# Optimization experiments

Measured on AMD Instinct MI355X. Metric: run time of the kernel, lower is better.

Reference implementation:

```python
import jax, jax.numpy as jnp
import numpy as np

HIDDEN = 2048
NUM_HEADS = 16
NUM_KV_HEADS = 4
HEAD_DIM = HIDDEN // NUM_HEADS  # 128
ROPE_THETA = 1000000.0
B, S = 2, 2048


def setup_inputs() -> dict:
    key = jax.random.key(0)
    ks = jax.random.split(key, 10)
    sc = 0.02
    return {
        "hidden_states": jax.random.normal(ks[0], (B, S, HIDDEN), jnp.float32),
        "position_ids": jnp.broadcast_to(jnp.arange(S, dtype=jnp.int32), (B, S)),
        "Wq": jax.random.normal(ks[1], (HIDDEN, NUM_HEADS * HEAD_DIM), jnp.float32) * sc,
        "bq": jnp.zeros((NUM_HEADS * HEAD_DIM,), jnp.float32),
        "Wk": jax.random.normal(ks[2], (HIDDEN, NUM_KV_HEADS * HEAD_DIM), jnp.float32) * sc,
        "bk": jnp.zeros((NUM_KV_HEADS * HEAD_DIM,), jnp.float32),
        "Wv": jax.random.normal(ks[3], (HIDDEN, NUM_KV_HEADS * HEAD_DIM), jnp.float32) * sc,
        "bv": jnp.zeros((NUM_KV_HEADS * HEAD_DIM,), jnp.float32),
        "Wo": jax.random.normal(ks[4], (NUM_HEADS * HEAD_DIM, HIDDEN), jnp.float32) * sc,
        "bo": jnp.zeros((HIDDEN,), jnp.float32),
    }


def _rope_cos_sin(position_ids, dtype):
    # inv_freq: [head_dim/2]
    inv_freq = 1.0 / (ROPE_THETA ** (jnp.arange(0, HEAD_DIM, 2, dtype=jnp.float32) / HEAD_DIM))
    freqs = position_ids.astype(jnp.float32)[:, :, None] * inv_freq[None, None, :]  # [B,S,d/2]
    emb = jnp.concatenate([freqs, freqs], axis=-1)  # [B,S,d]
    return jnp.cos(emb).astype(dtype), jnp.sin(emb).astype(dtype)


def _rotate_half(x):
    h = x.shape[-1] // 2
    return jnp.concatenate([-x[..., h:], x[..., :h]], axis=-1)


def _attention(hidden_states, position_ids, Wq, bq, Wk, bk, Wv, bv, Wo, bo):
    bsz, q_len, _ = hidden_states.shape
    q = (hidden_states @ Wq + bq).reshape(bsz, q_len, NUM_HEADS, HEAD_DIM).transpose(0, 2, 1, 3)
    k = (hidden_states @ Wk + bk).reshape(bsz, q_len, NUM_KV_HEADS, HEAD_DIM).transpose(0, 2, 1, 3)
    v = (hidden_states @ Wv + bv).reshape(bsz, q_len, NUM_KV_HEADS, HEAD_DIM).transpose(0, 2, 1, 3)

    cos, sin = _rope_cos_sin(position_ids, hidden_states.dtype)
    cos = cos[:, None, :, :]  # [B,1,S,d]
    sin = sin[:, None, :, :]
    q = q * cos + _rotate_half(q) * sin
    k = k * cos + _rotate_half(k) * sin

    # repeat_kv (GQA): [B,kvh,S,d] -> [B,H,S,d]
    n_rep = NUM_HEADS // NUM_KV_HEADS
    k = jnp.repeat(k, n_rep, axis=1)
    v = jnp.repeat(v, n_rep, axis=1)

    scale = 1.0 / jnp.sqrt(jnp.array(HEAD_DIM, hidden_states.dtype))
    scores = jnp.einsum('bhqd,bhkd->bhqk', q, k) * scale  # [B,H,S,S]
    causal = jnp.tril(jnp.ones((q_len, q_len), bool))
    scores = jnp.where(causal[None, None], scores, jnp.finfo(scores.dtype).min)
    probs = jax.nn.softmax(scores.astype(jnp.float32), axis=-1).astype(hidden_states.dtype)
    attn = jnp.einsum('bhqk,bhkd->bhqd', probs, v)
    attn = attn.transpose(0, 2, 1, 3).reshape(bsz, q_len, HIDDEN)
    return attn @ Wo + bo


def reference(hidden_states, position_ids, Wq, bq, Wk, bk, Wv, bv, Wo, bo):
    return _attention(hidden_states, position_ids, Wq, bq, Wk, bk, Wv, bv, Wo, bo)
```

## Files before the change

kernel.cpp:

```cpp
#include <hip/hip_runtime.h>
#include <cmath>

#define HIDDEN 2048
#define NH 16
#define NKV 4
#define HD 128
#define SEQ 2048
#define BATCH 2

typedef unsigned short ushort_t;
typedef short bf16x8 __attribute__((ext_vector_type(8)));
typedef float f32x4 __attribute__((ext_vector_type(4)));
typedef ushort_t u16x4 __attribute__((ext_vector_type(4)));

__device__ __forceinline__ ushort_t f2bf(float f) {
    union { float f; unsigned int u; } v; v.f = f;
    unsigned int r = v.u + 0x7fffu + ((v.u >> 16) & 1u);
    return (ushort_t)(r >> 16);
}
__device__ __forceinline__ ushort_t f2bf_trunc(float f) {
    union { float f; unsigned int u; } v; v.f = f;
    return (ushort_t)(v.u >> 16);
}

__device__ __forceinline__ f32x4 mfma16(bf16x8 a, bf16x8 b, f32x4 c) {
    return __builtin_amdgcn_mfma_f32_16x16x32_bf16(a, b, c, 0, 0, 0);
}

__device__ __forceinline__ void load_lds16(const void* g, void* l) {
    __builtin_amdgcn_global_load_lds((const __attribute__((address_space(1))) unsigned int*)g,
                                     (__attribute__((address_space(3))) unsigned int*)l,
                                     16, 0, 0);
}

__global__ __launch_bounds__(256) void convert_x(const float* __restrict__ x,
                                                 ushort_t* __restrict__ xb, int n4) {
    int g = blockIdx.x * 256 + threadIdx.x;
    if (g >= n4) return;
    float4 v = ((const float4*)x)[g];
    u16x4 o;
    o[0] = f2bf(v.x); o[1] = f2bf(v.y); o[2] = f2bf(v.z); o[3] = f2bf(v.w);
    ((u16x4*)xb)[g] = o;
}

__global__ __launch_bounds__(256) void transpose_all(const float* __restrict__ Wq,
                                                     const float* __restrict__ Wk,
                                                     const float* __restrict__ Wv,
                                                     const float* __restrict__ Wo,
                                                     ushort_t* __restrict__ WqkvT,
                                                     ushort_t* __restrict__ WoT) {
    const int z = blockIdx.z;
    const float* W;
    ushort_t* WT;
    int N;
    if (z == 0)      { W = Wq; WT = WqkvT;                        N = 2048; }
    else if (z == 1) { W = Wk; WT = WqkvT + 2048ull * 2048;       N = 512;  }
    else if (z == 2) { W = Wv; WT = WqkvT + 2560ull * 2048;       N = 512;  }
    else             { W = Wo; WT = WoT;                          N = 2048; }
    const int K = 2048;
    const int n0 = blockIdx.x * 64, k0 = blockIdx.y * 64;
    if (n0 >= N) return;
    __shared__ ushort_t T[64][72];
    const int t = threadIdx.x;
    for (int idx = t; idx < 64 * 16; idx += 256) {
        int r = idx >> 4, c4 = (idx & 15) << 2;
        float4 v = *(const float4*)&W[(size_t)(k0 + r) * N + n0 + c4];
        T[r][c4 + 0] = f2bf(v.x); T[r][c4 + 1] = f2bf(v.y);
        T[r][c4 + 2] = f2bf(v.z); T[r][c4 + 3] = f2bf(v.w);
    }
    __syncthreads();
    for (int idx = t; idx < 64 * 16; idx += 256) {
        int n = idx >> 4, kg = (idx & 15) << 2;
        u16x4 o;
        o[0] = T[kg + 0][n]; o[1] = T[kg + 1][n];
        o[2] = T[kg + 2][n]; o[3] = T[kg + 3][n];
        *(u16x4*)&WT[(size_t)(n0 + n) * K + k0 + kg] = o;
    }
}

template <int MODE, int BMH>
__global__ __launch_bounds__(512) void gemm256(const ushort_t* __restrict__ A,
                                               const ushort_t* __restrict__ Bt,
                                               const float* __restrict__ bias,
                                               const float* __restrict__ bias2,
                                               const float* __restrict__ bias3,
                                               void* __restrict__ out,
                                               void* __restrict__ out2,
                                               void* __restrict__ out3,
                                               int M, int N, int K,
                                               const int* __restrict__ posids) {
    constexpr int IM = 4 * BMH;
    __shared__ __align__(16) ushort_t Asb[2][BMH * 8192];
    __shared__ __align__(16) ushort_t Bsb[2][16384];
    const int tid = threadIdx.x;
    const int w = tid >> 6, lane = tid & 63, quad = lane >> 4, l16 = lane & 15;
    const int wr = w >> 2, wc = w & 3;
    const int m0 = blockIdx.y * (128 * BMH), n0 = blockIdx.x * 256;

    f32x4 acc[IM][4];
#pragma unroll
    for (int i = 0; i < IM; i++)
#pragma unroll
        for (int j = 0; j < 4; j++)
#pragma unroll
            for (int e = 0; e < 4; e++) acc[i][j][e] = 0.0f;

    const int lrow = lane >> 3;
    const int kh_s = ((lane >> 2) & 1) ^ ((lane >> 3) & 1);
    const int c_s  = (lane & 3) ^ ((lane >> 4) & 3);
    const int scol = kh_s * 32 + c_s * 8;

    auto stageA = [&](int t, int buf, int ha) {
        const ushort_t* g = A + (size_t)(m0 + ha * 128 + w * 16 + lrow) * K + t * 64 + scol;
        ushort_t* l = &Asb[buf][(ha * 128 + w * 16) * 64];
        load_lds16(g, l);
        load_lds16(g + (size_t)8 * K, l + 512);
    };
    auto stageB = [&](int t, int buf, int ha) {
        const ushort_t* g = Bt + (size_t)(n0 + ha * 128 + w * 16 + lrow) * K + t * 64 + scol;
        ushort_t* l = &Bsb[buf][(ha * 128 + w * 16) * 64];
        load_lds16(g, l);
        load_lds16(g + (size_t)8 * K, l + 512);
    };

    const int sw = (quad ^ ((l16 >> 1) & 3)) * 8;
    const int off0 = ((l16 & 1) ? 32 : 0) + sw;
    const int off1 = ((l16 & 1) ? 0 : 32) + sw;
    const int arow = (wr * (64 * BMH) + l16) * 64;
    const int brow = (wc * 16 + l16) * 64;

    const int nt = K >> 6;

    stageA(0, 0, 0);
    if constexpr (BMH == 2) stageA(0, 0, 1);
    stageB(0, 0, 0);
    stageB(0, 0, 1);
    asm volatile("s_waitcnt vmcnt(2)" ::: "memory");
    __builtin_amdgcn_s_barrier();
    __builtin_amdgcn_sched_barrier(0);

    bf16x8 a[IM];
    for (int u = 0; u < nt; ++u) {
        const int bu = u & 1, bn = bu ^ 1;
        const bool pf = (u + 1 < nt);
        const ushort_t* Ab = Asb[bu];
        const ushort_t* Bb = Bsb[bu];

#pragma unroll
        for (int i = 0; i < IM; i++) a[i] = *(const bf16x8*)&Ab[arow + i * 1024 + off0];
        bf16x8 b0 = *(const bf16x8*)&Bb[brow + off0];
        bf16x8 b1 = *(const bf16x8*)&Bb[brow + 4096 + off0];
        if (pf) { stageA(u + 1, bn, 0); asm volatile("s_waitcnt vmcnt(2)" ::: "memory"); }
        else    { asm volatile("s_waitcnt vmcnt(0)" ::: "memory"); }
        __builtin_amdgcn_s_barrier();
        __builtin_amdgcn_sched_barrier(0);
        __builtin_amdgcn_s_setprio(1);
#pragma unroll
        for (int i = 0; i < IM; i++) {
            acc[i][0] = mfma16(a[i], b0, acc[i][0]);
            acc[i][1] = mfma16(a[i], b1, acc[i][1]);
        }
        __builtin_amdgcn_s_setprio(0);
        __builtin_amdgcn_sched_barrier(0);
        __builtin_amdgcn_s_barrier();
        __builtin_amdgcn_sched_barrier(0);

        bf16x8 b2 = *(const bf16x8*)&Bb[brow + 8192 + off0];
        bf16x8 b3 = *(const bf16x8*)&Bb[brow + 12288 + off0];
        if (pf) {
            if constexpr (BMH == 2) stageA(u + 1, bn, 1);
            else                    stageB(u + 1, bn, 0);
        }
        __builtin_amdgcn_s_barrier();
        __builtin_amdgcn_sched_barrier(0);
        __builtin_amdgcn_s_setprio(1);
#pragma unroll
        for (int i = 0; i < IM; i++) {
            acc[i][2] = mfma16(a[i], b2, acc[i][2]);
            acc[i][3] = mfma16(a[i], b3, acc[i][3]);
        }
        __builtin_amdgcn_s_setprio(0);
        __builtin_amdgcn_sched_barrier(0);
        __builtin_amdgcn_s_barrier();
        __builtin_amdgcn_sched_barrier(0);

#pragma unroll
        for (int i = 0; i < IM; i++) a[i] = *(const bf16x8*)&Ab[arow + i * 1024 + off1];
        b0 = *(const bf16x8*)&Bb[brow + off1];
        b1 = *(const bf16x8*)&Bb[brow + 4096 + off1];
        if (pf) {
            if constexpr (BMH == 2) stageB(u + 1, bn, 0);
            else                    stageB(u + 1, bn, 1);
        }
        __builtin_amdgcn_s_barrier();
        __builtin_amdgcn_sched_barrier(0);
        __builtin_amdgcn_s_setprio(1);
#pragma unroll
        for (int i = 0; i < IM; i++) {
            acc[i][0] = mfma16(a[i], b0, acc[i][0]);
            acc[i][1] = mfma16(a[i], b1, acc[i][1]);
        }
        __builtin_amdgcn_s_setprio(0);
        __builtin_amdgcn_sched_barrier(0);
        __builtin_amdgcn_s_barrier();
        __builtin_amdgcn_sched_barrier(0);

        b2 = *(const bf16x8*)&Bb[brow + 8192 + off1];
        b3 = *(const bf16x8*)&Bb[brow + 12288 + off1];
        if (pf) {
            if constexpr (BMH == 2) stageB(u + 1, bn, 1);
            asm volatile("s_waitcnt vmcnt(2)" ::: "memory");
        }
        __builtin_amdgcn_s_barrier();
        __builtin_amdgcn_sched_barrier(0);
        __builtin_amdgcn_s_setprio(1);
#pragma unroll
        for (int i = 0; i < IM; i++) {
            acc[i][2] = mfma16(a[i], b2, acc[i][2]);
            acc[i][3] = mfma16(a[i], b3, acc[i][3]);
        }
        __builtin_amdgcn_s_setprio(0);
        __builtin_amdgcn_sched_barrier(0);
        __builtin_amdgcn_s_barrier();
        __builtin_amdgcn_sched_barrier(0);
    }

    if (MODE == 0) {
        float* O = (float*)out;
#pragma unroll
        for (int i = 0; i < IM; i++)
#pragma unroll
            for (int r = 0; r < 4; r++) {
                int row = m0 + wr * (64 * BMH) + i * 16 + quad * 4 + r;
#pragma unroll
                for (int j = 0; j < 4; j++) {
                    int col = n0 + (wc + 4 * j) * 16 + l16;
                    O[(size_t)row * N + col] = acc[i][j][r] + bias[col];
                }
            }
    } else {
        if (n0 < 2048) {
            ushort_t* O = (ushort_t*)out;
            const int h0 = n0 >> 7;
            const float scale = 0.08838834764831845f;
            const int dl = wc * 16 + l16;
            const float fr = __expf(-0.21586735246819178f * (float)dl);
#pragma unroll
            for (int i = 0; i < IM; i++)
#pragma unroll
                for (int r = 0; r < 4; r++) {
                    int row = m0 + wr * (64 * BMH) + i * 16 + quad * 4 + r;
                    int b = row >> 11, s = row & (SEQ - 1);
                    float pos = (float)posids[row];
                    float sn, cs;
                    __sincosf(pos * fr, &sn, &cs);
#pragma unroll
                    for (int p = 0; p < 2; p++) {
                        float x1 = acc[i][2 * p][r] + bias[n0 + p * 128 + dl];
                        float x2 = acc[i][2 * p + 1][r] + bias[n0 + p * 128 + dl + 64];
                        size_t obase = ((size_t)(b * NH + h0 + p) * SEQ + s) * HD;
                        O[obase + dl]      = f2bf((x1 * cs - x2 * sn) * scale);
                        O[obase + dl + 64] = f2bf((x2 * cs + x1 * sn) * scale);
                    }
                }
        } else if (n0 < 2560) {
            ushort_t* O = (ushort_t*)out2;
            const int n0k = n0 - 2048;
            const int h0 = n0k >> 7;
            const int dl = wc * 16 + l16;
            const float fr = __expf(-0.21586735246819178f * (float)dl);
#pragma unroll
            for (int i = 0; i < IM; i++)
#pragma unroll
                for (int r = 0; r < 4; r++) {
                    int row = m0 + wr * (64 * BMH) + i * 16 + quad * 4 + r;
                    int b = row >> 11, s = row & (SEQ - 1);
                    float pos = (float)posids[row];
                    float sn, cs;
                    __sincosf(pos * fr, &sn, &cs);
#pragma unroll
                    for (int p = 0; p < 2; p++) {
                        float x1 = acc[i][2 * p][r] + bias2[n0k + p * 128 + dl];
                        float x2 = acc[i][2 * p + 1][r] + bias2[n0k + p * 128 + dl + 64];
                        size_t obase = ((size_t)(b * NKV + h0 + p) * SEQ + s) * HD;
                        O[obase + dl]      = f2bf(x1 * cs - x2 * sn);
                        O[obase + dl + 64] = f2bf(x2 * cs + x1 * sn);
                    }
                }
        } else {
            ushort_t* O = (ushort_t*)out3;
            const int n0v = n0 - 2560;
#pragma unroll
            for (int i = 0; i < IM; i++)
#pragma unroll
                for (int r = 0; r < 4; r++) {
                    int row = m0 + wr * (64 * BMH) + i * 16 + quad * 4 + r;
                    int b = row >> 11, s = row & (SEQ - 1);
#pragma unroll
                    for (int j = 0; j < 4; j++) {
                        int ct = wc + 4 * j;
                        int h = (n0v >> 7) + (ct >> 3);
                        int d = (ct & 7) * 16 + l16;
                        float v = acc[i][j][r] + bias3[n0v + ct * 16 + l16];
                        O[((size_t)(b * NKV + h) * HD + d) * SEQ + s] = f2bf(v);
                    }
                }
        }
    }
}

__global__ __launch_bounds__(256) void flash(const ushort_t* __restrict__ Qr,
                                             const ushort_t* __restrict__ Kr,
                                             const ushort_t* __restrict__ Vt,
                                             ushort_t* __restrict__ Attn) {
    __shared__ __align__(16) ushort_t Ksh[2 * 4 * 64 * 32];
    __shared__ __align__(16) ushort_t Vsh[2 * 2 * 128 * 32];
    __shared__ __align__(16) ushort_t Ps[4 * 16 * 72];
    const int tid = threadIdx.x;
    const int w = tid >> 6, lane = tid & 63, quad = lane >> 4, l16 = lane & 15;
    const int x = blockIdx.x, h = blockIdx.y, b = blockIdx.z;
    const int qa = x, qb = 31 - x;
    const int nkt = qb + 1;
    const int hkv = h >> 2;
    const ushort_t* Kg = Kr + ((size_t)(b * NKV + hkv) * SEQ) * HD;
    const ushort_t* Vg = Vt + ((size_t)(b * NKV + hkv) * HD) * SEQ;

    const int p = lane >> 2;
    const int gc8 = (((lane & 3) ^ ((lane >> 3) & 3)) << 3);
    const ushort_t* kst = Kg + (size_t)p * HD + w * 32 + gc8;
    const ushort_t* vst = Vg + (size_t)((w & 1) * 64 + p) * SEQ + (w >> 1) * 32 + gc8;
    ushort_t* ksl = Ksh + w * 2048;
    ushort_t* vsl = Vsh + (w >> 1) * 4096 + (w & 1) * 2048;

    auto stage = [&](int bi, int kv0) {
        const ushort_t* gk = kst + (size_t)kv0 * HD;
        ushort_t* lk = ksl + bi * 8192;
        load_lds16(gk, lk);
        load_lds16(gk + (size_t)16 * HD, lk + 512);
        load_lds16(gk + (size_t)32 * HD, lk + 1024);
        load_lds16(gk + (size_t)48 * HD, lk + 1536);
        const ushort_t* gv = vst + kv0;
        ushort_t* lv = vsl + bi * 8192;
        load_lds16(gv, lv);
        load_lds16(gv + (size_t)16 * SEQ, lv + 512);
        load_lds16(gv + (size_t)32 * SEQ, lv + 1024);
        load_lds16(gv + (size_t)48 * SEQ, lv + 1536);
    };

    bf16x8 aq[2][4];
#pragma unroll
    for (int st = 0; st < 2; st++) {
        const int qst = st ? qb : qa;
        const size_t qrow = ((size_t)(b * NH + h) * SEQ + qst * 64 + w * 16 + l16) * HD;
#pragma unroll
        for (int kc = 0; kc < 4; kc++)
            aq[st][kc] = *(const bf16x8*)&Qr[qrow + kc * 32 + quad * 8];
    }

    f32x4 o[2][8];
#pragma unroll
    for (int st = 0; st < 2; st++)
#pragma unroll
        for (int j = 0; j < 8; j++)
#pragma unroll
            for (int e = 0; e < 4; e++) o[st][j][e] = 0.0f;
    f32x4 ls2[2];
#pragma unroll
    for (int st = 0; st < 2; st++)
        for (int e = 0; e < 4; e++) ls2[st][e] = 0.0f;
    bf16x8 ones;
#pragma unroll
    for (int e = 0; e < 8; e++) ones[e] = (short)0x3F80;

    ushort_t* Pw = &Ps[w * 16 * 72];
    const int rsw8 = ((l16 >> 1) & 3) << 3;

    stage(0, 0);
    asm volatile("s_waitcnt vmcnt(0)" ::: "memory");
    __builtin_amdgcn_s_barrier();

    for (int kt = 0; kt < nkt; kt++) {
        const int kv0 = kt * 64;
        const int cur = kt & 1;
        if (kt + 1 < nkt) {
            stage(cur ^ 1, kv0 + 64);
            asm volatile("s_waitcnt vmcnt(8)" ::: "memory");
        } else {
            asm volatile("s_waitcnt vmcnt(0)" ::: "memory");
        }
        __builtin_amdgcn_s_barrier();

        const ushort_t* Kb = Ksh + cur * 8192;
        const ushort_t* Vb = Vsh + cur * 8192;

#pragma unroll
        for (int st = 0; st < 2; st++) {
            const int qst = st ? qb : qa;
            if (st == 0 && kt > qa) continue;

            f32x4 sa[4];
#pragma unroll
            for (int nt = 0; nt < 4; nt++)
#pragma unroll
                for (int e = 0; e < 4; e++) sa[nt][e] = 0.0f;
#pragma unroll
            for (int kc = 0; kc < 4; kc++) {
#pragma unroll
                for (int nt = 0; nt < 4; nt++) {
                    bf16x8 bk = *(const bf16x8*)&Kb[kc * 2048 + nt * 512 + l16 * 32 +
                                                    ((quad * 8) ^ rsw8)];
                    sa[nt] = mfma16(aq[st][kc], bk, sa[nt]);
                }
            }

            if (kt == qst) {
#pragma unroll
                for (int nt = 0; nt < 4; nt++)
#pragma unroll
                    for (int r = 0; r < 4; r++) {
                        int kvg = kv0 + nt * 16 + l16;
                        int qg = qst * 64 + w * 16 + quad * 4 + r;
                        if (kvg > qg) sa[nt][r] = -1e30f;
                    }
            }

#pragma unroll
            for (int nt = 0; nt < 4; nt++)
#pragma unroll
                for (int r = 0; r < 4; r++)
                    Pw[(quad * 4 + r) * 72 + nt * 16 + l16] = f2bf_trunc(__expf(sa[nt][r]));

#pragma unroll
            for (int kc = 0; kc < 2; kc++) {
                bf16x8 ap = *(const bf16x8*)&Pw[l16 * 72 + kc * 32 + quad * 8];
                ls2[st] = mfma16(ap, ones, ls2[st]);
#pragma unroll
                for (int j = 0; j < 8; j++) {
                    bf16x8 bv = *(const bf16x8*)&Vb[kc * 4096 + (j * 16 + l16) * 32 +
                                                    ((quad * 8) ^ rsw8)];
                    o[st][j] = mfma16(ap, bv, o[st][j]);
                }
            }
        }
        asm volatile("s_barrier" ::: "memory");
    }

#pragma unroll
    for (int st = 0; st < 2; st++) {
        const int qst = st ? qb : qa;
#pragma unroll
        for (int r = 0; r < 4; r++) {
            float inv = 1.0f / ls2[st][r];
            int row = b * SEQ + qst * 64 + w * 16 + quad * 4 + r;
            size_t obase = (size_t)row * HIDDEN + h * HD;
#pragma unroll
            for (int j = 0; j < 8; j++) Attn[obase + j * 16 + l16] = f2bf(o[st][j][r] * inv);
        }
    }
}

extern "C" void kernel_launch(void* const* d_in, const int* in_sizes, int n_in,
                              void* d_out, int out_size, void* d_ws, size_t ws_size,
                              hipStream_t stream) {
    const float* hs = (const float*)d_in[0];
    const int* posids = (const int*)d_in[1];
    const float* Wq = (const float*)d_in[2];
    const float* bq = (const float*)d_in[3];
    const float* Wk = (const float*)d_in[4];
    const float* bk = (const float*)d_in[5];
    const float* Wv = (const float*)d_in[6];
    const float* bv = (const float*)d_in[7];
    const float* Wo = (const float*)d_in[8];
    const float* bo = (const float*)d_in[9];
    float* out = (float*)d_out;

    char* ws = (char*)d_ws;
    size_t off = 0;
    auto alloc = [&](size_t bytes) {
        char* p = ws + off;
        off += (bytes + 255) & ~(size_t)255;
        return p;
    };
    ushort_t* Xb     = (ushort_t*)alloc(4096ull * 2048 * 2);
    ushort_t* WqkvT  = (ushort_t*)alloc(3072ull * 2048 * 2);
    ushort_t* WoT    = (ushort_t*)alloc(2048ull * 2048 * 2);
    ushort_t* Qr     = (ushort_t*)alloc((size_t)BATCH * NH * SEQ * HD * 2);
    ushort_t* Kr     = (ushort_t*)alloc((size_t)BATCH * NKV * SEQ * HD * 2);
    ushort_t* Vtr    = (ushort_t*)alloc((size_t)BATCH * NKV * HD * SEQ * 2);
    ushort_t* Attn   = (ushort_t*)alloc(4096ull * 2048 * 2);

    convert_x<<<4096 * 2048 / 4 / 256, 256, 0, stream>>>(hs, Xb, 4096 * 2048 / 4);
    transpose_all<<<dim3(32, 32, 4), 256, 0, stream>>>(Wq, Wk, Wv, Wo, WqkvT, WoT);

    gemm256<2, 2><<<dim3(12, 16), 512, 0, stream>>>(Xb, WqkvT, bq, bk, bv,
                                                    Qr, Kr, Vtr, 4096, 3072, 2048, posids);

    flash<<<dim3(16, NH, BATCH), 256, 0, stream>>>(Qr, Kr, Vtr, Attn);

    gemm256<0, 1><<<dim3(8, 32), 512, 0, stream>>>(Attn, WoT, bo, nullptr, nullptr,
                                                   out, nullptr, nullptr, 4096, 2048, 2048, nullptr);
}
```

Before: 314.9 us.

## Split GEMM LDS tiles into K-half planes and merge prep kernels into one launch

The GEMM shared-memory layout changes from 64-wide rows with a swizzled half selector to two separate 32-column planes per buffer. Each lane now loads one 16-byte chunk from each K half of the same row, with an XOR swizzle on the column slot. The goal is to cut LDS bank conflicts and simplify the fragment addressing. Separately, the x conversion and the weight transposes are fused into a single prep launch using extra z-slices, which saves one kernel launch. The risk is new bank-conflict patterns if the swizzle does not line up with the read pattern.

Measured after the change: 298.7 us. -5.1%, faster.

```diff
diff --git a/kernel.cpp b/kernel.cpp
--- a/kernel.cpp
+++ b/kernel.cpp
@@ -33,23 +33,25 @@
                                      16, 0, 0);
 }
 
-__global__ __launch_bounds__(256) void convert_x(const float* __restrict__ x,
-                                                 ushort_t* __restrict__ xb, int n4) {
-    int g = blockIdx.x * 256 + threadIdx.x;
-    if (g >= n4) return;
-    float4 v = ((const float4*)x)[g];
-    u16x4 o;
-    o[0] = f2bf(v.x); o[1] = f2bf(v.y); o[2] = f2bf(v.z); o[3] = f2bf(v.w);
-    ((u16x4*)xb)[g] = o;
-}
-
-__global__ __launch_bounds__(256) void transpose_all(const float* __restrict__ Wq,
-                                                     const float* __restrict__ Wk,
-                                                     const float* __restrict__ Wv,
-                                                     const float* __restrict__ Wo,
-                                                     ushort_t* __restrict__ WqkvT,
-                                                     ushort_t* __restrict__ WoT) {
+
+__global__ __launch_bounds__(256) void prep(const float* __restrict__ Wq,
+                                            const float* __restrict__ Wk,
+                                            const float* __restrict__ Wv,
+                                            const float* __restrict__ Wo,
+                                            ushort_t* __restrict__ WqkvT,
+                                            ushort_t* __restrict__ WoT,
+                                            const float* __restrict__ hs,
+                                            ushort_t* __restrict__ Xb) {
     const int z = blockIdx.z;
+    const int t = threadIdx.x;
+    if (z >= 4) {
+        int g = (((z - 4) * 32 + blockIdx.y) * 32 + blockIdx.x) * 256 + t;
+        float4 v = ((const float4*)hs)[g];
+        u16x4 o;
+        o[0] = f2bf(v.x); o[1] = f2bf(v.y); o[2] = f2bf(v.z); o[3] = f2bf(v.w);
+        ((u16x4*)Xb)[g] = o;
+        return;
+    }
     const float* W;
     ushort_t* WT;
     int N;
@@ -61,7 +63,6 @@
     const int n0 = blockIdx.x * 64, k0 = blockIdx.y * 64;
     if (n0 >= N) return;
     __shared__ ushort_t T[64][72];
-    const int t = threadIdx.x;
     for (int idx = t; idx < 64 * 16; idx += 256) {
         int r = idx >> 4, c4 = (idx & 15) << 2;
         float4 v = *(const float4*)&W[(size_t)(k0 + r) * N + n0 + c4];
@@ -90,8 +91,10 @@
                                                int M, int N, int K,
                                                const int* __restrict__ posids) {
     constexpr int IM = 4 * BMH;
-    __shared__ __align__(16) ushort_t Asb[2][BMH * 8192];
-    __shared__ __align__(16) ushort_t Bsb[2][16384];
+    constexpr int APL = BMH * 128 * 32;
+    constexpr int BPL = 256 * 32;
+    __shared__ __align__(16) ushort_t Asb[2 * 2 * APL];
+    __shared__ __align__(16) ushort_t Bsb[2 * 2 * BPL];
     const int tid = threadIdx.x;
     const int w = tid >> 6, lane = tid & 63, quad = lane >> 4, l16 = lane & 15;
     const int wr = w >> 2, wc = w & 3;
@@ -105,29 +108,25 @@
 #pragma unroll
             for (int e = 0; e < 4; e++) acc[i][j][e] = 0.0f;
 
-    const int lrow = lane >> 3;
-    const int kh_s = ((lane >> 2) & 1) ^ ((lane >> 3) & 1);
-    const int c_s  = (lane & 3) ^ ((lane >> 4) & 3);
-    const int scol = kh_s * 32 + c_s * 8;
+    const int srow = lane >> 2;
+    const int gc8 = (((lane & 3) ^ ((lane >> 3) & 3)) << 3);
 
     auto stageA = [&](int t, int buf, int ha) {
-        const ushort_t* g = A + (size_t)(m0 + ha * 128 + w * 16 + lrow) * K + t * 64 + scol;
-        ushort_t* l = &Asb[buf][(ha * 128 + w * 16) * 64];
+        const ushort_t* g = A + (size_t)(m0 + ha * 128 + w * 16 + srow) * K + t * 64 + gc8;
+        ushort_t* l = &Asb[buf * 2 * APL + (ha * 128 + w * 16) * 32];
         load_lds16(g, l);
-        load_lds16(g + (size_t)8 * K, l + 512);
+        load_lds16(g + 32, l + APL);
     };
     auto stageB = [&](int t, int buf, int ha) {
-        const ushort_t* g = Bt + (size_t)(n0 + ha * 128 + w * 16 + lrow) * K + t * 64 + scol;
-        ushort_t* l = &Bsb[buf][(ha * 128 + w * 16) * 64];
+        const ushort_t* g = Bt + (size_t)(n0 + ha * 128 + w * 16 + srow) * K + t * 64 + gc8;
+        ushort_t* l = &Bsb[buf * 2 * BPL + (ha * 128 + w * 16) * 32];
         load_lds16(g, l);
-        load_lds16(g + (size_t)8 * K, l + 512);
+        load_lds16(g + 32, l + BPL);
     };
 
-    const int sw = (quad ^ ((l16 >> 1) & 3)) * 8;
-    const int off0 = ((l16 & 1) ? 32 : 0) + sw;
-    const int off1 = ((l16 & 1) ? 0 : 32) + sw;
-    const int arow = (wr * (64 * BMH) + l16) * 64;
-    const int brow = (wc * 16 + l16) * 64;
+    const int slot = ((quad ^ ((l16 >> 1) & 3)) << 3);
+    const int arow = (wr * (64 * BMH) + l16) * 32 + slot;
+    const int brow = (wc * 16 + l16) * 32 + slot;
 
     const int nt = K >> 6;
 
@@ -143,13 +142,15 @@
     for (int u = 0; u < nt; ++u) {
         const int bu = u & 1, bn = bu ^ 1;
         const bool pf = (u + 1 < nt);
-        const ushort_t* Ab = Asb[bu];
-        const ushort_t* Bb = Bsb[bu];
-
-#pragma unroll
-        for (int i = 0; i < IM; i++) a[i] = *(const bf16x8*)&Ab[arow + i * 1024 + off0];
-        bf16x8 b0 = *(const bf16x8*)&Bb[brow + off0];
-        bf16x8 b1 = *(const bf16x8*)&Bb[brow + 4096 + off0];
+        const ushort_t* Ap0 = &Asb[bu * 2 * APL];
+        const ushort_t* Ap1 = Ap0 + APL;
+        const ushort_t* Bp0 = &Bsb[bu * 2 * BPL];
+        const ushort_t* Bp1 = Bp0 + BPL;
+
+#pragma unroll
+        for (int i = 0; i < IM; i++) a[i] = *(const bf16x8*)&Ap0[arow + i * 512];
+        bf16x8 b0 = *(const bf16x8*)&Bp0[brow];
+        bf16x8 b1 = *(const bf16x8*)&Bp0[brow + 2048];
         if (pf) { stageA(u + 1, bn, 0); asm volatile("s_waitcnt vmcnt(2)" ::: "memory"); }
         else    { asm volatile("s_waitcnt vmcnt(0)" ::: "memory"); }
         __builtin_amdgcn_s_barrier();
@@ -165,8 +166,8 @@
         __builtin_amdgcn_s_barrier();
         __builtin_amdgcn_sched_barrier(0);
 
-        bf16x8 b2 = *(const bf16x8*)&Bb[brow + 8192 + off0];
-        bf16x8 b3 = *(const bf16x8*)&Bb[brow + 12288 + off0];
+        bf16x8 b2 = *(const bf16x8*)&Bp0[brow + 4096];
+        bf16x8 b3 = *(const bf16x8*)&Bp0[brow + 6144];
         if (pf) {
             if constexpr (BMH == 2) stageA(u + 1, bn, 1);
             else                    stageB(u + 1, bn, 0);
@@ -185,9 +186,9 @@
         __builtin_amdgcn_sched_barrier(0);
 
 #pragma unroll
-        for (int i = 0; i < IM; i++) a[i] = *(const bf16x8*)&Ab[arow + i * 1024 + off1];
-        b0 = *(const bf16x8*)&Bb[brow + off1];
-        b1 = *(const bf16x8*)&Bb[brow + 4096 + off1];
+        for (int i = 0; i < IM; i++) a[i] = *(const bf16x8*)&Ap1[arow + i * 512];
+        b0 = *(const bf16x8*)&Bp1[brow];
+        b1 = *(const bf16x8*)&Bp1[brow + 2048];
         if (pf) {
             if constexpr (BMH == 2) stageB(u + 1, bn, 0);
             else                    stageB(u + 1, bn, 1);
@@ -205,8 +206,8 @@
         __builtin_amdgcn_s_barrier();
         __builtin_amdgcn_sched_barrier(0);
 
-        b2 = *(const bf16x8*)&Bb[brow + 8192 + off1];
-        b3 = *(const bf16x8*)&Bb[brow + 12288 + off1];
+        b2 = *(const bf16x8*)&Bp1[brow + 4096];
+        b3 = *(const bf16x8*)&Bp1[brow + 6144];
         if (pf) {
             if constexpr (BMH == 2) stageB(u + 1, bn, 1);
             asm volatile("s_waitcnt vmcnt(2)" ::: "memory");
@@ -489,8 +490,7 @@
     ushort_t* Vtr    = (ushort_t*)alloc((size_t)BATCH * NKV * HD * SEQ * 2);
     ushort_t* Attn   = (ushort_t*)alloc(4096ull * 2048 * 2);
 
-    convert_x<<<4096 * 2048 / 4 / 256, 256, 0, stream>>>(hs, Xb, 4096 * 2048 / 4);
-    transpose_all<<<dim3(32, 32, 4), 256, 0, stream>>>(Wq, Wk, Wv, Wo, WqkvT, WoT);
+    prep<<<dim3(32, 32, 12), 256, 0, stream>>>(Wq, Wk, Wv, Wo, WqkvT, WoT, hs, Xb);
 
     gemm256<2, 2><<<dim3(12, 16), 512, 0, stream>>>(Xb, WqkvT, bq, bk, bv,
                                                     Qr, Kr, Vtr, 4096, 3072, 2048, posids);
```
